# Optimization experiments

Measured on AMD Instinct MI355X. Metric: run time of the kernel, lower is better.

## Reference

```python
import jax, jax.numpy as jnp
import numpy as np

N_NODES = 10000
N_EDGES = 160000
HIDDEN = 256
HEADS = 8
LN_EPS = 1e-5


def setup_inputs() -> dict:
    key = jax.random.key(0)
    ks = jax.random.split(key, 8)
    s = 1.0 / np.sqrt(HIDDEN)
    return {
        "node_embeddings": jax.random.normal(ks[0], (1, N_NODES, HIDDEN), jnp.float32),
        "edge_index": jax.random.randint(ks[1], (2, N_EDGES), 0, N_NODES, dtype=jnp.int32),
        "Wq": jax.random.normal(ks[2], (HIDDEN, HIDDEN), jnp.float32) * s,
        "Wk": jax.random.normal(ks[3], (HIDDEN, HIDDEN), jnp.float32) * s,
        "Wv": jax.random.normal(ks[4], (HIDDEN, HIDDEN), jnp.float32) * s,
        "Wo": jax.random.normal(ks[5], (HIDDEN, HIDDEN), jnp.float32) * s,
        "ln_gamma": jnp.ones((HIDDEN,), jnp.float32),
        "ln_beta": jnp.zeros((HIDDEN,), jnp.float32),
    }


def reference(node_embeddings, edge_index, Wq, Wk, Wv, Wo, ln_gamma, ln_beta):
    B, N, Dm = node_embeddings.shape
    H = HEADS
    hd = Dm // H
    scale = 1.0 / np.sqrt(hd)

    def heads(x):  # [B,N,Dm] -> [B,H,N,hd]
        return x.reshape(B, N, H, hd).transpose(0, 2, 1, 3)

    Q = heads(node_embeddings @ Wq)
    K = heads(node_embeddings @ Wk)
    V = heads(node_embeddings @ Wv)

    src, dst = edge_index[0], edge_index[1]
    Qe = Q[:, :, src, :]           # [B,H,E,hd]
    Ke = K[:, :, dst, :]
    Ve = V[:, :, dst, :]

    scores = jnp.einsum('bhed,bhed->bhe', Qe, Ke) * scale   # [B,H,E]
    s_t = scores.transpose(2, 0, 1)                          # [E,B,H]
    smax = jax.ops.segment_max(s_t, src, num_segments=N)    # [N,B,H]
    ex = jnp.exp(s_t - smax[src])                            # [E,B,H]
    denom = jax.ops.segment_sum(ex, src, num_segments=N)    # [N,B,H]
    attn = ex / denom[src]                                   # scatter-softmax weights

    wV = attn[..., None] * Ve.transpose(2, 0, 1, 3)          # [E,B,H,hd]
    agg = jax.ops.segment_sum(wV, src, num_segments=N)      # [N,B,H,hd]
    attn_out = agg.transpose(1, 0, 2, 3).reshape(B, N, Dm)   # [B,N,Dm]

    out = attn_out @ Wo
    x = out + node_embeddings
    mu = jnp.mean(x, axis=-1, keepdims=True)
    var = jnp.mean((x - mu) ** 2, axis=-1, keepdims=True)
    return (x - mu) * jax.lax.rsqrt(var + LN_EPS) * ln_gamma + ln_beta
```

## Files before the change

kernel.cpp:

```cpp
#include <hip/hip_runtime.h>

#define NN 10000
#define NE 160000
#define DM 256
#define CAP 96
#define LN_EPSF 1e-5f
#define SCALEF 0.17677669529663687f

typedef unsigned short u16;
typedef __attribute__((ext_vector_type(4))) u16 u16x4;
typedef __attribute__((ext_vector_type(8))) u16 u16x8;
typedef __attribute__((ext_vector_type(4))) float f32x4;
typedef __attribute__((ext_vector_type(8))) short short8;

__device__ __forceinline__ float b2f(u16 u) { return __uint_as_float(((unsigned)u) << 16); }
__device__ __forceinline__ u16 f2b(float f) {
    unsigned u = __float_as_uint(f);
    return (u16)((u + 0x7fffu + ((u >> 16) & 1u)) >> 16);
}
__device__ __forceinline__ int clampi(int v) { return v < 0 ? 0 : (v >= NN ? NN - 1 : v); }

__global__ void k_fill_zero_f32(float* __restrict__ o, int n) {
    int i = blockIdx.x * 256 + threadIdx.x;
    if (i < n) o[i] = 0.f;
}

__global__ void k_prep(const float* __restrict__ Wq, const float* __restrict__ Wk,
                       const float* __restrict__ Wv, const float* __restrict__ Wo,
                       u16* __restrict__ Wt, int* __restrict__ cnt) {
    int id = blockIdx.x * 256 + threadIdx.x;
    if (id < NN) cnt[id] = 0;
    int m = id >> 16;
    int rc = id & 65535;
    int r = rc >> 8, c = rc & 255;
    const float* W = (m == 0) ? Wq : (m == 1) ? Wk : (m == 2) ? Wv : Wo;
    Wt[m * 65536 + c * 256 + r] = f2b(W[r * 256 + c]);
}

__global__ __launch_bounds__(256) void k_qkv_bucket(const float* __restrict__ X, const u16* __restrict__ Wt,
                                                    u16* __restrict__ Q, u16* __restrict__ KV,
                                                    const int* __restrict__ EI, int* __restrict__ cnt,
                                                    int* __restrict__ buck) {
    constexpr int ALS = 264;
    __shared__ u16 AtL[32 * ALS];
    if (blockIdx.y == 3) {
        int e0 = blockIdx.x * 512 + threadIdx.x;
#pragma unroll
        for (int h = 0; h < 2; h++) {
            int e = e0 + h * 256;
            if (e < NE) {
                int s = clampi(EI[e]);
                int slot = atomicAdd(&cnt[s], 1);
                if (slot < CAP) buck[s * CAP + slot] = clampi(EI[NE + e]);
            }
        }
        return;
    }
    const int t = threadIdx.x;
    const int w = t >> 6, l = t & 63, quad = l >> 4, m16 = l & 15;
    const int mat = blockIdx.y;
    const u16* Wm = Wt + mat * 65536;
    const int node0 = blockIdx.x * 32;
    {
        const int arow = t >> 3, ac32 = (t & 7) * 32;
        const int anode = node0 + arow;
#pragma unroll
        for (int j = 0; j < 4; j++) {
            u16x8 av = {0, 0, 0, 0, 0, 0, 0, 0};
            if (anode < NN) {
                const float* xp = X + (size_t)anode * DM + ac32 + j * 8;
                f32x4 a0 = *(const f32x4*)(xp);
                f32x4 a1 = *(const f32x4*)(xp + 4);
                av[0] = f2b(a0[0]); av[1] = f2b(a0[1]); av[2] = f2b(a0[2]); av[3] = f2b(a0[3]);
                av[4] = f2b(a1[0]); av[5] = f2b(a1[1]); av[6] = f2b(a1[2]); av[7] = f2b(a1[3]);
            }
            *(u16x8*)(AtL + arow * ALS + ac32 + j * 8) = av;
        }
    }
    __syncthreads();
    f32x4 acc[2][4];
#pragma unroll
    for (int i = 0; i < 2; i++)
#pragma unroll
        for (int j = 0; j < 4; j++) acc[i][j] = (f32x4){0.f, 0.f, 0.f, 0.f};
    short8 bc[4];
#pragma unroll
    for (int ct = 0; ct < 4; ct++)
        bc[ct] = *(const short8*)(Wm + (size_t)(w * 64 + ct * 16 + m16) * DM + quad * 8);
#pragma unroll
    for (int k0 = 0; k0 < DM; k0 += 32) {
        short8 bn[4];
        if (k0 + 32 < DM) {
#pragma unroll
            for (int ct = 0; ct < 4; ct++)
                bn[ct] = *(const short8*)(Wm + (size_t)(w * 64 + ct * 16 + m16) * DM + (k0 + 32) + quad * 8);
        }
        short8 a[2];
#pragma unroll
        for (int rt = 0; rt < 2; rt++)
            a[rt] = *(const short8*)(AtL + (rt * 16 + m16) * ALS + k0 + quad * 8);
#pragma unroll
        for (int rt = 0; rt < 2; rt++)
#pragma unroll
            for (int ct = 0; ct < 4; ct++)
                acc[rt][ct] = __builtin_amdgcn_mfma_f32_16x16x32_bf16(a[rt], bc[ct], acc[rt][ct], 0, 0, 0);
        if (k0 + 32 < DM) {
#pragma unroll
            for (int ct = 0; ct < 4; ct++) bc[ct] = bn[ct];
        }
    }
#pragma unroll
    for (int rt = 0; rt < 2; rt++) {
#pragma unroll
        for (int ct = 0; ct < 4; ct++) {
            int col = w * 64 + ct * 16 + m16;
#pragma unroll
            for (int r = 0; r < 4; r++) {
                int node = node0 + rt * 16 + quad * 4 + r;
                if (node < NN) {
                    u16 v = f2b(acc[rt][ct][r]);
                    if (mat == 0) Q[(size_t)node * DM + col] = v;
                    else KV[(size_t)node * 512 + col + ((mat == 2) ? 256 : 0)] = v;
                }
            }
        }
    }
}

#define UPD8(mm, ss, AA, vv, p, msk) do {                 \
    float nm_ = fmaxf(mm, p);                             \
    float al_ = __expf(mm - nm_);                         \
    float pe_ = __expf(p - nm_) * (msk);                  \
    ss = ss * al_ + pe_;                                  \
    _Pragma("unroll")                                     \
    for (int d_ = 0; d_ < 8; d_++)                        \
        AA[d_] = AA[d_] * al_ + pe_ * b2f(vv[d_]);        \
    mm = nm_;                                             \
} while (0)

__global__ __launch_bounds__(128) void k_edge(const u16* __restrict__ Q, const u16* __restrict__ KV,
                                              const int* __restrict__ cnt, const int* __restrict__ buck,
                                              u16* __restrict__ attn) {
    const int t = threadIdx.x;
    const int wv = t >> 6, l = t & 63;
    const int hl = l & 31, up = l >> 5;
    const int node = blockIdx.x * 2 + wv;
    int deg = cnt[node];
    if (deg > CAP) deg = CAP;
    const int* bl = buck + node * CAP;
    u16x8 q8 = *(const u16x8*)(Q + (size_t)node * DM + hl * 8);
    float qf[8];
#pragma unroll
    for (int d = 0; d < 8; d++) qf[d] = b2f(q8[d]) * SCALEF;
    float mm[4], ss[4], AA[4][8];
#pragma unroll
    for (int j = 0; j < 4; j++) {
        mm[j] = -3.0e38f;
        ss[j] = 0.f;
#pragma unroll
        for (int d = 0; d < 8; d++) AA[j][d] = 0.f;
    }
    int i = 0;
    int deg8 = deg & ~7;
    for (; i < deg8; i += 8) {
        int4 ea = *(const int4*)(bl + i);
        int4 eb = *(const int4*)(bl + i + 4);
        int dst[4];
        dst[0] = up ? ea.y : ea.x;
        dst[1] = up ? ea.w : ea.z;
        dst[2] = up ? eb.y : eb.x;
        dst[3] = up ? eb.w : eb.z;
        u16x8 kk[4], vv[4];
#pragma unroll
        for (int j = 0; j < 4; j++) {
            const u16* row = KV + (size_t)dst[j] * 512;
            kk[j] = *(const u16x8*)(row + hl * 8);
            vv[j] = *(const u16x8*)(row + 256 + hl * 8);
        }
        float p[4];
#pragma unroll
        for (int j = 0; j < 4; j++) {
            float s = 0.f;
#pragma unroll
            for (int d = 0; d < 8; d++) s += qf[d] * b2f(kk[j][d]);
            p[j] = s;
        }
#pragma unroll
        for (int j = 0; j < 4; j++) p[j] += __shfl_xor(p[j], 1, 64);
#pragma unroll
        for (int j = 0; j < 4; j++) p[j] += __shfl_xor(p[j], 2, 64);
#pragma unroll
        for (int j = 0; j < 4; j++) UPD8(mm[j], ss[j], AA[j], vv[j], p[j], 1.0f);
    }
    for (; i < deg; i += 2) {
        int jj = i + up;
        float msk = (jj < deg) ? 1.f : 0.f;
        int dst = bl[(jj < deg) ? jj : i];
        const u16* row = KV + (size_t)dst * 512;
        u16x8 kk = *(const u16x8*)(row + hl * 8);
        u16x8 vv = *(const u16x8*)(row + 256 + hl * 8);
        float p = 0.f;
#pragma unroll
        for (int d = 0; d < 8; d++) p += qf[d] * b2f(kk[d]);
        p += __shfl_xor(p, 1, 64);
        p += __shfl_xor(p, 2, 64);
        UPD8(mm[0], ss[0], AA[0], vv, p, msk);
    }
    float nm = fmaxf(fmaxf(mm[0], mm[1]), fmaxf(mm[2], mm[3]));
    float S = 0.f, O[8];
#pragma unroll
    for (int d = 0; d < 8; d++) O[d] = 0.f;
#pragma unroll
    for (int j = 0; j < 4; j++) {
        float wj = __expf(mm[j] - nm);
        S += ss[j] * wj;
#pragma unroll
        for (int d = 0; d < 8; d++) O[d] += AA[j][d] * wj;
    }
    float om = __shfl_xor(nm, 32, 64);
    float oS = __shfl_xor(S, 32, 64);
    float oO[8];
#pragma unroll
    for (int d = 0; d < 8; d++) oO[d] = __shfl_xor(O[d], 32, 64);
    float fm = fmaxf(nm, om);
    float wa = __expf(nm - fm), wb = __expf(om - fm);
    float S2 = S * wa + oS * wb;
    float inv = (S2 > 0.f) ? 1.f / S2 : 0.f;
    if (up == 0) {
        u16x8 o;
#pragma unroll
        for (int d = 0; d < 8; d++) o[d] = f2b((O[d] * wa + oO[d] * wb) * inv);
        *(u16x8*)(attn + (size_t)node * DM + hl * 8) = o;
    }
}

__global__ __launch_bounds__(256) void k_gemm_out_ln(const u16* __restrict__ In, const u16* __restrict__ WoT,
                                                     const float* __restrict__ X, const float* __restrict__ g,
                                                     const float* __restrict__ b, float* __restrict__ out) {
    constexpr int ALS = 264;
    __shared__ u16 AtL[32 * ALS];
    __shared__ float gbuf[256], bbuf[256];
    __shared__ float redS[4][32], redQ[4][32], muS[32], rsS[32];
    const int t = threadIdx.x;
    gbuf[t] = g[t];
    bbuf[t] = b[t];
    const int w = t >> 6, l = t & 63, quad = l >> 4, m16 = l & 15;
    const int node0 = blockIdx.x * 32;
    {
        const int arow = t >> 3, ac32 = (t & 7) * 32;
        const int anode = node0 + arow;
#pragma unroll
        for (int j = 0; j < 4; j++) {
            u16x8 av = {0, 0, 0, 0, 0, 0, 0, 0};
            if (anode < NN) av = *(const u16x8*)(In + (size_t)anode * DM + ac32 + j * 8);
            *(u16x8*)(AtL + arow * ALS + ac32 + j * 8) = av;
        }
    }
    __syncthreads();
    f32x4 acc[2][4];
#pragma unroll
    for (int i = 0; i < 2; i++)
#pragma unroll
        for (int j = 0; j < 4; j++) acc[i][j] = (f32x4){0.f, 0.f, 0.f, 0.f};
    short8 bc[4];
#pragma unroll
    for (int ct = 0; ct < 4; ct++)
        bc[ct] = *(const short8*)(WoT + (size_t)(w * 64 + ct * 16 + m16) * DM + quad * 8);
#pragma unroll
    for (int k0 = 0; k0 < DM; k0 += 32) {
        short8 bn[4];
        if (k0 + 32 < DM) {
#pragma unroll
            for (int ct = 0; ct < 4; ct++)
                bn[ct] = *(const short8*)(WoT + (size_t)(w * 64 + ct * 16 + m16) * DM + (k0 + 32) + quad * 8);
        }
        short8 a[2];
#pragma unroll
        for (int rt = 0; rt < 2; rt++)
            a[rt] = *(const short8*)(AtL + (rt * 16 + m16) * ALS + k0 + quad * 8);
#pragma unroll
        for (int rt = 0; rt < 2; rt++)
#pragma unroll
            for (int ct = 0; ct < 4; ct++)
                acc[rt][ct] = __builtin_amdgcn_mfma_f32_16x16x32_bf16(a[rt], bc[ct], acc[rt][ct], 0, 0, 0);
        if (k0 + 32 < DM) {
#pragma unroll
            for (int ct = 0; ct < 4; ct++) bc[ct] = bn[ct];
        }
    }
#pragma unroll
    for (int rt = 0; rt < 2; rt++)
#pragma unroll
        for (int ct = 0; ct < 4; ct++) {
            int col = w * 64 + ct * 16 + m16;
#pragma unroll
            for (int r = 0; r < 4; r++) {
                int node = node0 + rt * 16 + quad * 4 + r;
                float x = (node < NN) ? X[(size_t)node * DM + col] : 0.f;
                acc[rt][ct][r] += x;
            }
        }
#pragma unroll
    for (int rt = 0; rt < 2; rt++) {
#pragma unroll
        for (int r = 0; r < 4; r++) {
            float p1 = acc[rt][0][r] + acc[rt][1][r] + acc[rt][2][r] + acc[rt][3][r];
            float p2 = acc[rt][0][r] * acc[rt][0][r] + acc[rt][1][r] * acc[rt][1][r] +
                       acc[rt][2][r] * acc[rt][2][r] + acc[rt][3][r] * acc[rt][3][r];
#pragma unroll
            for (int o = 1; o < 16; o <<= 1) {
                p1 += __shfl_xor(p1, o, 64);
                p2 += __shfl_xor(p2, o, 64);
            }
            if (m16 == 0) {
                int row = rt * 16 + quad * 4 + r;
                redS[w][row] = p1;
                redQ[w][row] = p2;
            }
        }
    }
    __syncthreads();
    if (t < 32) {
        float s1t = redS[0][t] + redS[1][t] + redS[2][t] + redS[3][t];
        float s2t = redQ[0][t] + redQ[1][t] + redQ[2][t] + redQ[3][t];
        float mmv = s1t * (1.f / DM);
        float var = s2t * (1.f / DM) - mmv * mmv;
        muS[t] = mmv;
        rsS[t] = rsqrtf(var + LN_EPSF);
    }
    __syncthreads();
#pragma unroll
    for (int rt = 0; rt < 2; rt++)
#pragma unroll
        for (int ct = 0; ct < 4; ct++) {
            int col = w * 64 + ct * 16 + m16;
#pragma unroll
            for (int r = 0; r < 4; r++) {
                int row = rt * 16 + quad * 4 + r;
                int node = node0 + row;
                if (node < NN)
                    out[(size_t)node * DM + col] = (acc[rt][ct][r] - muS[row]) * rsS[row] * gbuf[col] + bbuf[col];
            }
        }
}

extern "C" void kernel_launch(void* const* d_in, const int* in_sizes, int n_in,
                              void* d_out, int out_size, void* d_ws, size_t ws_size,
                              hipStream_t stream) {
    (void)in_sizes; (void)n_in;
    const float* X  = (const float*)d_in[0];
    const int*   EI = (const int*)d_in[1];
    const float* Wq = (const float*)d_in[2];
    const float* Wk = (const float*)d_in[3];
    const float* Wv = (const float*)d_in[4];
    const float* Wo = (const float*)d_in[5];
    const float* g  = (const float*)d_in[6];
    const float* be = (const float*)d_in[7];

    const size_t SWT  = (size_t)4 * 65536 * 2;
    const size_t SKV  = (size_t)NN * 512 * 2;
    const size_t SCNT = (size_t)NN * 4;
    const size_t SBK  = (size_t)NN * CAP * 4;
    const size_t SQB  = (size_t)NN * DM * 2;
    const size_t SAT  = (size_t)NN * DM * 2;
    const size_t need = SWT + SKV + SCNT + SBK + SQB + SAT;
    if (ws_size < need) {
        k_fill_zero_f32<<<(out_size + 255) / 256, 256, 0, stream>>>((float*)d_out, out_size);
        return;
    }
    char* p = (char*)d_ws;
    u16* Wt   = (u16*)p; p += SWT;
    u16* KVb  = (u16*)p; p += SKV;
    int* cnt  = (int*)p; p += SCNT;
    int* buck = (int*)p; p += SBK;
    u16* Qb   = (u16*)p; p += SQB;
    u16* attn = (u16*)p; p += SAT;

    k_prep<<<1024, 256, 0, stream>>>(Wq, Wk, Wv, Wo, Wt, cnt);
    k_qkv_bucket<<<dim3(313, 4), 256, 0, stream>>>(X, Wt, Qb, KVb, EI, cnt, buck);
    k_edge<<<NN / 2, 128, 0, stream>>>(Qb, KVb, cnt, buck, attn);
    k_gemm_out_ln<<<313, 256, 0, stream>>>(attn, Wt + 3 * 65536, X, g, be, (float*)d_out);
}
```

Baseline: 147.8 us.

## Retile QKV and output GEMMs to 64-row tiles with LDS-staged weight K-slices

Measured after the change: 147.7 us. No clear change (-0.1%).

```diff
diff --git a/kernel.cpp b/kernel.cpp
--- a/kernel.cpp
+++ b/kernel.cpp
@@ -41,76 +41,68 @@
                                                     u16* __restrict__ Q, u16* __restrict__ KV,
                                                     const int* __restrict__ EI, int* __restrict__ cnt,
                                                     int* __restrict__ buck) {
-    constexpr int ALS = 264;
-    __shared__ u16 AtL[32 * ALS];
+    constexpr int AS = 40;
+    __shared__ u16 At[64 * AS];
+    __shared__ u16 Bt[256 * AS];
     if (blockIdx.y == 3) {
-        int e0 = blockIdx.x * 512 + threadIdx.x;
-#pragma unroll
-        for (int h = 0; h < 2; h++) {
-            int e = e0 + h * 256;
-            if (e < NE) {
-                int s = clampi(EI[e]);
-                int slot = atomicAdd(&cnt[s], 1);
-                if (slot < CAP) buck[s * CAP + slot] = clampi(EI[NE + e]);
-            }
+        int e = blockIdx.x * 256 + threadIdx.x;
+        if (e < NE) {
+            int s = clampi(EI[e]);
+            int slot = atomicAdd(&cnt[s], 1);
+            if (slot < CAP) buck[s * CAP + slot] = clampi(EI[NE + e]);
         }
         return;
     }
+    if (blockIdx.x >= 157) return;
     const int t = threadIdx.x;
     const int w = t >> 6, l = t & 63, quad = l >> 4, m16 = l & 15;
     const int mat = blockIdx.y;
     const u16* Wm = Wt + mat * 65536;
-    const int node0 = blockIdx.x * 32;
-    {
-        const int arow = t >> 3, ac32 = (t & 7) * 32;
-        const int anode = node0 + arow;
-#pragma unroll
-        for (int j = 0; j < 4; j++) {
-            u16x8 av = {0, 0, 0, 0, 0, 0, 0, 0};
-            if (anode < NN) {
-                const float* xp = X + (size_t)anode * DM + ac32 + j * 8;
-                f32x4 a0 = *(const f32x4*)(xp);
-                f32x4 a1 = *(const f32x4*)(xp + 4);
-                av[0] = f2b(a0[0]); av[1] = f2b(a0[1]); av[2] = f2b(a0[2]); av[3] = f2b(a0[3]);
-                av[4] = f2b(a1[0]); av[5] = f2b(a1[1]); av[6] = f2b(a1[2]); av[7] = f2b(a1[3]);
-            }
-            *(u16x8*)(AtL + arow * ALS + ac32 + j * 8) = av;
-        }
-    }
-    __syncthreads();
-    f32x4 acc[2][4];
-#pragma unroll
-    for (int i = 0; i < 2; i++)
+    const int node0 = blockIdx.x * 64;
+    f32x4 acc[4][4];
+#pragma unroll
+    for (int i = 0; i < 4; i++)
 #pragma unroll
         for (int j = 0; j < 4; j++) acc[i][j] = (f32x4){0.f, 0.f, 0.f, 0.f};
-    short8 bc[4];
-#pragma unroll
-    for (int ct = 0; ct < 4; ct++)
-        bc[ct] = *(const short8*)(Wm + (size_t)(w * 64 + ct * 16 + m16) * DM + quad * 8);
-#pragma unroll
+    const int arow = t >> 2, ac8 = (t & 3) * 8;
     for (int k0 = 0; k0 < DM; k0 += 32) {
-        short8 bn[4];
-        if (k0 + 32 < DM) {
+        u16x8 av = {0, 0, 0, 0, 0, 0, 0, 0};
+        int anode = node0 + arow;
+        if (anode < NN) {
+            const float* xp = X + (size_t)anode * DM + k0 + ac8;
+            f32x4 a0 = *(const f32x4*)(xp);
+            f32x4 a1 = *(const f32x4*)(xp + 4);
+            av[0] = f2b(a0[0]); av[1] = f2b(a0[1]); av[2] = f2b(a0[2]); av[3] = f2b(a0[3]);
+            av[4] = f2b(a1[0]); av[5] = f2b(a1[1]); av[6] = f2b(a1[2]); av[7] = f2b(a1[3]);
+        }
+        *(u16x8*)(At + arow * AS + ac8) = av;
+        const u16* bsrc = Wm + t * DM + k0;
+        u16x8 b0 = *(const u16x8*)(bsrc);
+        u16x8 b1 = *(const u16x8*)(bsrc + 8);
+        u16x8 b2 = *(const u16x8*)(bsrc + 16);
+        u16x8 b3 = *(const u16x8*)(bsrc + 24);
+        u16* bd = Bt + t * AS;
+        *(u16x8*)(bd) = b0;
+        *(u16x8*)(bd + 8) = b1;
+        *(u16x8*)(bd + 16) = b2;
+        *(u16x8*)(bd + 24) = b3;
+        __syncthreads();
+        short8 a[4], b[4];
+#pragma unroll
+        for (int rt = 0; rt < 4; rt++)
+            a[rt] = *(const short8*)(At + (rt * 16 + m16) * AS + quad * 8);
+#pragma unroll
+        for (int ct = 0; ct < 4; ct++)
+            b[ct] = *(const short8*)(Bt + (w * 64 + ct * 16 + m16) * AS + quad * 8);
+#pragma unroll
+        for (int rt = 0; rt < 4; rt++)
 #pragma unroll
             for (int ct = 0; ct < 4; ct++)
-                bn[ct] = *(const short8*)(Wm + (size_t)(w * 64 + ct * 16 + m16) * DM + (k0 + 32) + quad * 8);
-        }
-        short8 a[2];
-#pragma unroll
-        for (int rt = 0; rt < 2; rt++)
-            a[rt] = *(const short8*)(AtL + (rt * 16 + m16) * ALS + k0 + quad * 8);
-#pragma unroll
-        for (int rt = 0; rt < 2; rt++)
-#pragma unroll
-            for (int ct = 0; ct < 4; ct++)
-                acc[rt][ct] = __builtin_amdgcn_mfma_f32_16x16x32_bf16(a[rt], bc[ct], acc[rt][ct], 0, 0, 0);
-        if (k0 + 32 < DM) {
-#pragma unroll
-            for (int ct = 0; ct < 4; ct++) bc[ct] = bn[ct];
-        }
-    }
-#pragma unroll
-    for (int rt = 0; rt < 2; rt++) {
+                acc[rt][ct] = __builtin_amdgcn_mfma_f32_16x16x32_bf16(a[rt], b[ct], acc[rt][ct], 0, 0, 0);
+        __syncthreads();
+    }
+#pragma unroll
+    for (int rt = 0; rt < 4; rt++) {
 #pragma unroll
         for (int ct = 0; ct < 4; ct++) {
             int col = w * 64 + ct * 16 + m16;
@@ -237,59 +229,55 @@
 __global__ __launch_bounds__(256) void k_gemm_out_ln(const u16* __restrict__ In, const u16* __restrict__ WoT,
                                                      const float* __restrict__ X, const float* __restrict__ g,
                                                      const float* __restrict__ b, float* __restrict__ out) {
-    constexpr int ALS = 264;
-    __shared__ u16 AtL[32 * ALS];
+    constexpr int AS = 40;
+    __shared__ u16 At[64 * AS];
+    __shared__ u16 Bt[256 * AS];
     __shared__ float gbuf[256], bbuf[256];
-    __shared__ float redS[4][32], redQ[4][32], muS[32], rsS[32];
+    __shared__ float redS[4][64], redQ[4][64];
+    __shared__ float muS[64], rsS[64];
     const int t = threadIdx.x;
     gbuf[t] = g[t];
     bbuf[t] = b[t];
     const int w = t >> 6, l = t & 63, quad = l >> 4, m16 = l & 15;
-    const int node0 = blockIdx.x * 32;
-    {
-        const int arow = t >> 3, ac32 = (t & 7) * 32;
-        const int anode = node0 + arow;
-#pragma unroll
-        for (int j = 0; j < 4; j++) {
-            u16x8 av = {0, 0, 0, 0, 0, 0, 0, 0};
-            if (anode < NN) av = *(const u16x8*)(In + (size_t)anode * DM + ac32 + j * 8);
-            *(u16x8*)(AtL + arow * ALS + ac32 + j * 8) = av;
-        }
-    }
-    __syncthreads();
-    f32x4 acc[2][4];
-#pragma unroll
-    for (int i = 0; i < 2; i++)
+    const int node0 = blockIdx.x * 64;
+    f32x4 acc[4][4];
+#pragma unroll
+    for (int i = 0; i < 4; i++)
 #pragma unroll
         for (int j = 0; j < 4; j++) acc[i][j] = (f32x4){0.f, 0.f, 0.f, 0.f};
-    short8 bc[4];
-#pragma unroll
-    for (int ct = 0; ct < 4; ct++)
-        bc[ct] = *(const short8*)(WoT + (size_t)(w * 64 + ct * 16 + m16) * DM + quad * 8);
-#pragma unroll
+    const int arow = t >> 2, ac8 = (t & 3) * 8;
     for (int k0 = 0; k0 < DM; k0 += 32) {
-        short8 bn[4];
-        if (k0 + 32 < DM) {
+        u16x8 av = {0, 0, 0, 0, 0, 0, 0, 0};
+        int anode = node0 + arow;
+        if (anode < NN) av = *(const u16x8*)(In + (size_t)anode * DM + k0 + ac8);
+        *(u16x8*)(At + arow * AS + ac8) = av;
+        const u16* bsrc = WoT + t * DM + k0;
+        u16x8 b0 = *(const u16x8*)(bsrc);
+        u16x8 b1 = *(const u16x8*)(bsrc + 8);
+        u16x8 b2 = *(const u16x8*)(bsrc + 16);
+        u16x8 b3 = *(const u16x8*)(bsrc + 24);
+        u16* bd = Bt + t * AS;
+        *(u16x8*)(bd) = b0;
+        *(u16x8*)(bd + 8) = b1;
+        *(u16x8*)(bd + 16) = b2;
+        *(u16x8*)(bd + 24) = b3;
+        __syncthreads();
+        short8 a[4], bf[4];
+#pragma unroll
+        for (int rt = 0; rt < 4; rt++)
+            a[rt] = *(const short8*)(At + (rt * 16 + m16) * AS + quad * 8);
+#pragma unroll
+        for (int ct = 0; ct < 4; ct++)
+            bf[ct] = *(const short8*)(Bt + (w * 64 + ct * 16 + m16) * AS + quad * 8);
+#pragma unroll
+        for (int rt = 0; rt < 4; rt++)
 #pragma unroll
             for (int ct = 0; ct < 4; ct++)
-                bn[ct] = *(const short8*)(WoT + (size_t)(w * 64 + ct * 16 + m16) * DM + (k0 + 32) + quad * 8);
-        }
-        short8 a[2];
-#pragma unroll
-        for (int rt = 0; rt < 2; rt++)
-            a[rt] = *(const short8*)(AtL + (rt * 16 + m16) * ALS + k0 + quad * 8);
-#pragma unroll
-        for (int rt = 0; rt < 2; rt++)
-#pragma unroll
-            for (int ct = 0; ct < 4; ct++)
-                acc[rt][ct] = __builtin_amdgcn_mfma_f32_16x16x32_bf16(a[rt], bc[ct], acc[rt][ct], 0, 0, 0);
-        if (k0 + 32 < DM) {
-#pragma unroll
-            for (int ct = 0; ct < 4; ct++) bc[ct] = bn[ct];
-        }
-    }
-#pragma unroll
-    for (int rt = 0; rt < 2; rt++)
+                acc[rt][ct] = __builtin_amdgcn_mfma_f32_16x16x32_bf16(a[rt], bf[ct], acc[rt][ct], 0, 0, 0);
+        __syncthreads();
+    }
+#pragma unroll
+    for (int rt = 0; rt < 4; rt++)
 #pragma unroll
         for (int ct = 0; ct < 4; ct++) {
             int col = w * 64 + ct * 16 + m16;
@@ -301,7 +289,7 @@
             }
         }
 #pragma unroll
-    for (int rt = 0; rt < 2; rt++) {
+    for (int rt = 0; rt < 4; rt++) {
 #pragma unroll
         for (int r = 0; r < 4; r++) {
             float p1 = acc[rt][0][r] + acc[rt][1][r] + acc[rt][2][r] + acc[rt][3][r];
@@ -320,17 +308,17 @@
         }
     }
     __syncthreads();
-    if (t < 32) {
+    if (t < 64) {
         float s1t = redS[0][t] + redS[1][t] + redS[2][t] + redS[3][t];
         float s2t = redQ[0][t] + redQ[1][t] + redQ[2][t] + redQ[3][t];
-        float mmv = s1t * (1.f / DM);
-        float var = s2t * (1.f / DM) - mmv * mmv;
-        muS[t] = mmv;
+        float mm = s1t * (1.f / DM);
+        float var = s2t * (1.f / DM) - mm * mm;
+        muS[t] = mm;
         rsS[t] = rsqrtf(var + LN_EPSF);
     }
     __syncthreads();
 #pragma unroll
-    for (int rt = 0; rt < 2; rt++)
+    for (int rt = 0; rt < 4; rt++)
 #pragma unroll
         for (int ct = 0; ct < 4; ct++) {
             int col = w * 64 + ct * 16 + m16;
@@ -359,11 +347,10 @@
 
     const size_t SWT  = (size_t)4 * 65536 * 2;
     const size_t SKV  = (size_t)NN * 512 * 2;
+    const size_t SAT  = (size_t)NN * DM * 2;
     const size_t SCNT = (size_t)NN * 4;
     const size_t SBK  = (size_t)NN * CAP * 4;
-    const size_t SQB  = (size_t)NN * DM * 2;
-    const size_t SAT  = (size_t)NN * DM * 2;
-    const size_t need = SWT + SKV + SCNT + SBK + SQB + SAT;
+    const size_t need = SWT + SKV + SAT + SCNT + SBK;
     if (ws_size < need) {
         k_fill_zero_f32<<<(out_size + 255) / 256, 256, 0, stream>>>((float*)d_out, out_size);
         return;
@@ -371,13 +358,13 @@
     char* p = (char*)d_ws;
     u16* Wt   = (u16*)p; p += SWT;
     u16* KVb  = (u16*)p; p += SKV;
+    u16* attn = (u16*)p; p += SAT;
     int* cnt  = (int*)p; p += SCNT;
     int* buck = (int*)p; p += SBK;
-    u16* Qb   = (u16*)p; p += SQB;
-    u16* attn = (u16*)p; p += SAT;
+    u16* Qb = (u16*)d_out;
 
     k_prep<<<1024, 256, 0, stream>>>(Wq, Wk, Wv, Wo, Wt, cnt);
-    k_qkv_bucket<<<dim3(313, 4), 256, 0, stream>>>(X, Wt, Qb, KVb, EI, cnt, buck);
+    k_qkv_bucket<<<dim3(625, 4), 256, 0, stream>>>(X, Wt, Qb, KVb, EI, cnt, buck);
     k_edge<<<NN / 2, 128, 0, stream>>>(Qb, KVb, cnt, buck, attn);
-    k_gemm_out_ln<<<313, 256, 0, stream>>>(attn, Wt + 3 * 65536, X, g, be, (float*)d_out);
-}
+    k_gemm_out_ln<<<157, 256, 0, stream>>>(attn, Wt + 3 * 65536, X, g, be, (float*)d_out);
+}
```
